# Optimization experiments

Hardware: AMD Instinct MI355X
Metric: run time of the kernel (lower is better)

Reference implementation:

```python
import jax, jax.numpy as jnp
import numpy as np

B, N = 8, 4096
LOCAL_DIM, GLOBAL_DIM, HIDDEN_DIM = 512, 128, 256


def setup_inputs() -> dict:
    key = jax.random.key(0)
    ks = jax.random.split(key, 10)
    def lin(kw, fan_in, fan_out):
        # torch nn.Linear default init: U(-1/sqrt(fan_in), 1/sqrt(fan_in))
        bound = 1.0 / np.sqrt(fan_in)
        W = jax.random.uniform(kw, (fan_in, fan_out), jnp.float32, -bound, bound)
        return W
    x = jax.random.normal(ks[0], (B, N, LOCAL_DIM), jnp.float32)
    g = jax.random.normal(ks[1], (B, 1, GLOBAL_DIM), jnp.float32)
    return {
        "x": x,
        "g": g,
        "Wq": lin(ks[2], LOCAL_DIM, HIDDEN_DIM),
        "bq": jax.random.uniform(ks[3], (HIDDEN_DIM,), jnp.float32, -1/np.sqrt(LOCAL_DIM), 1/np.sqrt(LOCAL_DIM)),
        "Wk": lin(ks[4], GLOBAL_DIM, HIDDEN_DIM),
        "bk": jax.random.uniform(ks[5], (HIDDEN_DIM,), jnp.float32, -1/np.sqrt(GLOBAL_DIM), 1/np.sqrt(GLOBAL_DIM)),
        "Wv": lin(ks[6], GLOBAL_DIM, HIDDEN_DIM),
        "bv": jax.random.uniform(ks[7], (HIDDEN_DIM,), jnp.float32, -1/np.sqrt(GLOBAL_DIM), 1/np.sqrt(GLOBAL_DIM)),
        "Wo": lin(ks[8], HIDDEN_DIM, LOCAL_DIM),
        "bo": jax.random.uniform(ks[9], (LOCAL_DIM,), jnp.float32, -1/np.sqrt(HIDDEN_DIM), 1/np.sqrt(HIDDEN_DIM)),
    }


def reference(x, g, Wq, bq, Wk, bk, Wv, bv, Wo, bo):
    # x: (B, N, local_dim); g: (B, 1, global_dim)
    Bsz, Npts, _ = x.shape
    # g.repeat(1, N, 1) == broadcast of the single global token along N
    g_exp = jnp.broadcast_to(g, (Bsz, Npts, g.shape[-1]))
    Q = x @ Wq + bq          # (B, N, H)
    K = g_exp @ Wk + bk      # (B, N, H) -- all rows identical per batch
    V = g_exp @ Wv + bv      # (B, N, H)
    scale = jnp.sqrt(jnp.asarray(HIDDEN_DIM, x.dtype))
    scores = jnp.einsum('bnh,bmh->bnm', Q, K) / scale   # (B, N, N)
    weights = jax.nn.softmax(scores, axis=-1)
    attended = jnp.einsum('bnm,bmh->bnh', weights, V)   # (B, N, H)
    return attended @ Wo + bo                           # (B, N, local_dim)
```

## Files before the change

### kernel.cpp

```cpp
#include <hip/hip_runtime.h>


#define BATCH      8
#define NPTS       4096
#define LOCAL_DIM  512
#define GLOBAL_DIM 128
#define HIDDEN_DIM 256

__global__ void cross_attn_rows(const float* __restrict__ g,
                                const float* __restrict__ Wv,
                                const float* __restrict__ bv,
                                const float* __restrict__ Wo,
                                const float* __restrict__ bo,
                                float* __restrict__ rows) {
    __shared__ float gsh[GLOBAL_DIM];
    __shared__ float Vsh[HIDDEN_DIM];
    __shared__ float partial[8][32];

    const int b  = blockIdx.x >> 4;
    const int jc = blockIdx.x & 15;
    const int t  = threadIdx.x;

    if (t < GLOBAL_DIM) gsh[t] = g[b * GLOBAL_DIM + t];
    __syncthreads();

    {
        float acc = bv[t];
        #pragma unroll 16
        for (int d = 0; d < GLOBAL_DIM; ++d)
            acc += gsh[d] * Wv[d * HIDDEN_DIM + t];
        Vsh[t] = acc;
    }
    __syncthreads();

    {
        const int j  = jc * 32 + (t & 31);
        const int h0 = (t >> 5) * 32;
        float p = 0.f;
        #pragma unroll
        for (int hh = 0; hh < 32; ++hh) {
            const int h = h0 + hh;
            p += Vsh[h] * Wo[h * LOCAL_DIM + j];
        }
        partial[t >> 5][t & 31] = p;
    }
    __syncthreads();

    if (t < 32) {
        const int j = jc * 32 + t;
        float r = bo[j];
        #pragma unroll
        for (int q = 0; q < 8; ++q) r += partial[q][t];
        rows[b * LOCAL_DIM + j] = r;
    }
}

__global__ void cross_attn_bcast(const float4* __restrict__ rows4,
                                 float4* __restrict__ out4) {
    const long long total  = (long long)BATCH * NPTS * (LOCAL_DIM / 4);
    const long long stride = (long long)gridDim.x * blockDim.x;
    long long idx = (long long)blockIdx.x * blockDim.x + threadIdx.x;

    const int j4 = (int)(idx & (LOCAL_DIM / 4 - 1));

    for (long long t = idx; t < total; t += stride) {
        const int b = (int)(t >> 19);
        out4[t] = rows4[b * (LOCAL_DIM / 4) + j4];
    }
}

extern "C" void kernel_launch(void* const* d_in, const int* in_sizes, int n_in,
                              void* d_out, int out_size, void* d_ws, size_t ws_size,
                              hipStream_t stream) {
    const float* g  = (const float*)d_in[1];
    const float* Wv = (const float*)d_in[6];
    const float* bv = (const float*)d_in[7];
    const float* Wo = (const float*)d_in[8];
    const float* bo = (const float*)d_in[9];

    float* rows = (float*)d_ws;

    cross_attn_rows<<<BATCH * 16, 256, 0, stream>>>(g, Wv, bv, Wo, bo, rows);

    cross_attn_bcast<<<4096, 256, 0, stream>>>((const float4*)rows,
                                               (float4*)d_out);
}
```

Before: 126.1 us.

## Fuse row computation and broadcast into one kernel with nontemporal stores

Merges the V/output-row computation and the broadcast write into a single kernel. Each block recomputes V, computes a 64-column slice of the output row into shared memory, and writes it across 512 points using nontemporal vector stores. This removes the second launch and the workspace round trip, at the cost of redundant per-block recomputation and fewer, longer-running blocks.

```diff
diff --git a/kernel.cpp b/kernel.cpp
--- a/kernel.cpp
+++ b/kernel.cpp
@@ -7,18 +7,24 @@
 #define GLOBAL_DIM 128
 #define HIDDEN_DIM 256
 
-__global__ void cross_attn_rows(const float* __restrict__ g,
-                                const float* __restrict__ Wv,
-                                const float* __restrict__ bv,
-                                const float* __restrict__ Wo,
-                                const float* __restrict__ bo,
-                                float* __restrict__ rows) {
-    __shared__ float gsh[GLOBAL_DIM];
-    __shared__ float Vsh[HIDDEN_DIM];
-    __shared__ float partial[8][32];
+typedef float vfloat4 __attribute__((ext_vector_type(4)));
 
-    const int b  = blockIdx.x >> 4;
-    const int jc = blockIdx.x & 15;
+__global__ __launch_bounds__(256) void cross_attn_fused(
+        const float* __restrict__ g,
+        const float* __restrict__ Wv,
+        const float* __restrict__ bv,
+        const float* __restrict__ Wo,
+        const float* __restrict__ bo,
+        vfloat4* __restrict__ out4) {
+    __shared__ float   gsh[GLOBAL_DIM];
+    __shared__ float   Vsh[HIDDEN_DIM];
+    __shared__ float   partial[4][64];
+    __shared__ vfloat4 row4sh[16];
+
+    const int blk = blockIdx.x;
+    const int b  = blk >> 6;
+    const int jc = (blk >> 3) & 7;
+    const int nc = blk & 7;
     const int t  = threadIdx.x;
 
     if (t < GLOBAL_DIM) gsh[t] = g[b * GLOBAL_DIM + t];
@@ -34,38 +40,34 @@
     __syncthreads();
 
     {
-        const int j  = jc * 32 + (t & 31);
-        const int h0 = (t >> 5) * 32;
+        const int j  = jc * 64 + (t & 63);
+        const int h0 = (t >> 6) * 64;
         float p = 0.f;
-        #pragma unroll
-        for (int hh = 0; hh < 32; ++hh) {
+        #pragma unroll 8
+        for (int hh = 0; hh < 64; ++hh) {
             const int h = h0 + hh;
             p += Vsh[h] * Wo[h * LOCAL_DIM + j];
         }
-        partial[t >> 5][t & 31] = p;
+        partial[t >> 6][t & 63] = p;
     }
     __syncthreads();
 
-    if (t < 32) {
-        const int j = jc * 32 + t;
-        float r = bo[j];
+    if (t < 64) {
+        float r = bo[jc * 64 + t];
         #pragma unroll
-        for (int q = 0; q < 8; ++q) r += partial[q][t];
-        rows[b * LOCAL_DIM + j] = r;
+        for (int q = 0; q < 4; ++q) r += partial[q][t];
+        ((float*)row4sh)[t] = r;
     }
-}
+    __syncthreads();
 
-__global__ void cross_attn_bcast(const float4* __restrict__ rows4,
-                                 float4* __restrict__ out4) {
-    const long long total  = (long long)BATCH * NPTS * (LOCAL_DIM / 4);
-    const long long stride = (long long)gridDim.x * blockDim.x;
-    long long idx = (long long)blockIdx.x * blockDim.x + threadIdx.x;
+    const vfloat4 rv = row4sh[t & 15];
+    const int   j4   = jc * 16 + (t & 15);
+    const int   nlan = t >> 4;
+    const int   base = (b * NPTS + nc * 512 + nlan) * (LOCAL_DIM / 4) + j4;
 
-    const int j4 = (int)(idx & (LOCAL_DIM / 4 - 1));
-
-    for (long long t = idx; t < total; t += stride) {
-        const int b = (int)(t >> 19);
-        out4[t] = rows4[b * (LOCAL_DIM / 4) + j4];
+    #pragma unroll 8
+    for (int it = 0; it < 32; ++it) {
+        __builtin_nontemporal_store(rv, out4 + base + it * 16 * (LOCAL_DIM / 4));
     }
 }
 
@@ -78,10 +80,6 @@
     const float* Wo = (const float*)d_in[8];
     const float* bo = (const float*)d_in[9];
 
-    float* rows = (float*)d_ws;
-
-    cross_attn_rows<<<BATCH * 16, 256, 0, stream>>>(g, Wv, bv, Wo, bo, rows);
-
-    cross_attn_bcast<<<4096, 256, 0, stream>>>((const float4*)rows,
-                                               (float4*)d_out);
+    cross_attn_fused<<<512, 256, 0, stream>>>(g, Wv, bv, Wo, bo,
+                                              (vfloat4*)d_out);
 }
```

Result: slower. 129.0 us (+2.3%).
